# Kernel tuning notes

Hardware: AMD Instinct MI355X
Metric: run time of the kernel (lower is better)

## Reference

```python
import jax, jax.numpy as jnp
import numpy as np

B, T_ENC, E, T_DEC, N_MELS, H, A = 32, 256, 512, 200, 80, 1024, 128


def setup_inputs() -> dict:
    key = jax.random.key(0)
    ks = jax.random.split(key, 20)
    rn = lambda k, s, sc: (jax.random.normal(k, s, jnp.float32) * sc)
    return {
        "inputs": rn(ks[0], (B, T_ENC, E), 1.0),
        "padded_mels": rn(ks[1], (B, N_MELS, T_DEC), 1.0),
        "W_enc": rn(ks[2], (E, A), 0.04),
        "W_q": rn(ks[3], (H, A), 0.03),
        "conv_w": rn(ks[4], (32, 1, 31), 0.18),
        "conv_b": jnp.zeros((32,), jnp.float32),
        "W_loc": rn(ks[5], (32, A), 0.18),
        "v_e": rn(ks[6], (A,), 0.09),
        "pw1": rn(ks[7], (N_MELS, 256), 0.11),
        "pb1": jnp.zeros((256,), jnp.float32),
        "pw2": rn(ks[8], (256, 256), 0.06),
        "pb2": jnp.zeros((256,), jnp.float32),
        "Wi1": rn(ks[9], (256 + E, 4 * H), 0.03),
        "Wh1": rn(ks[10], (H, 4 * H), 0.03),
        "bl1": jnp.zeros((4 * H,), jnp.float32),
        "Wi2": rn(ks[11], (H, 4 * H), 0.03),
        "Wh2": rn(ks[12], (H, 4 * H), 0.03),
        "bl2": jnp.zeros((4 * H,), jnp.float32),
        "Wp": rn(ks[13], (H + E, N_MELS), 0.025),
        "bp": jnp.zeros((N_MELS,), jnp.float32),
    }


def _lstm_cell(x, h, c, Wi, Wh, b):
    g = x @ Wi + h @ Wh + b
    i, f, gg, o = jnp.split(g, 4, axis=-1)
    c = jax.nn.sigmoid(f) * c + jax.nn.sigmoid(i) * jnp.tanh(gg)
    h = jax.nn.sigmoid(o) * jnp.tanh(c)
    return h, c


def reference(inputs, padded_mels, W_enc, W_q, conv_w, conv_b, W_loc, v_e,
              pw1, pb1, pw2, pb2, Wi1, Wh1, bl1, Wi2, Wh2, bl2, Wp, bp):
    b, t_enc, e = inputs.shape
    n_mels, t_dec = padded_mels.shape[1], padded_mels.shape[2]
    proc_enc = inputs @ W_enc  # [B, T_enc, A]
    # teacher forcing: prepend go frame, use frames 0..T_dec-1 as inputs
    go = jnp.zeros((b, n_mels, 1), inputs.dtype)
    prev_mels = jnp.moveaxis(jnp.concatenate([go, padded_mels], axis=-1)[:, :, :-1], -1, 0)  # [T_dec,B,80]

    def step(carry, prev_mel):
        h1, c1, h2, c2, ctx, aw_cum = carry
        # prenet (dropout omitted: eval/deterministic reference)
        x = jax.nn.relu(prev_mel @ pw1 + pb1)
        x = jax.nn.relu(x @ pw2 + pb2)
        # 2-layer LSTM on [prenet, prev context]
        lstm_in = jnp.concatenate([x, ctx], axis=-1)
        h1n, c1n = _lstm_cell(lstm_in, h1, c1, Wi1, Wh1, bl1)
        h2n, c2n = _lstm_cell(h1n, h2, c2, Wi2, Wh2, bl2)
        # location-sensitive attention
        q = h2n @ W_q  # [B, A]
        loc = jax.lax.conv_general_dilated(aw_cum[:, None, :], conv_w, (1,), "SAME",
                                           dimension_numbers=("NCH", "OIH", "NCH"))
        loc = loc + conv_b[None, :, None]
        loc = jnp.swapaxes(loc, 1, 2) @ W_loc  # [B, T_enc, A]
        energies = jnp.tanh(q[:, None, :] + loc + proc_enc) @ v_e  # [B, T_enc]
        aw = jax.nn.softmax(energies, axis=1)
        ctx_n = jnp.einsum("bt,bte->be", aw, inputs)
        out = jnp.concatenate([h2n, ctx_n], axis=-1) @ Wp + bp  # [B, 80]
        return (h1n, c1n, h2n, c2n, ctx_n, aw_cum + aw), out

    z = lambda *s: jnp.zeros(s, inputs.dtype)
    carry0 = (z(b, H), z(b, H), z(b, H), z(b, H), z(b, e), z(b, t_enc))
    _, mels = jax.lax.scan(step, carry0, prev_mels)
    return mels  # [T_dec, B, 80]
```

## Files before the change

kernel.cpp:

```cpp
#include <hip/hip_runtime.h>
#include <hip/hip_fp16.h>

#define BB   32
#define TENC 256
#define EE   512
#define TDEC 200
#define NM   80
#define HH   1024
#define AA   128
#define GG   4096
#define K1   1792
#define K2   2048

#define NGRP  16
#define GRPSZ 16

typedef _Float16 h8v  __attribute__((ext_vector_type(8)));
typedef float    f32x4 __attribute__((ext_vector_type(4)));

__device__ __forceinline__ float sigf(float x){ return 1.0f/(1.0f + __expf(-x)); }
__device__ __forceinline__ float tanhfast(float x){ return 1.0f - 2.0f/(1.0f + __expf(2.0f*x)); }

__device__ __forceinline__ unsigned short h2b(float f){
    _Float16 h = (_Float16)f; unsigned short u; __builtin_memcpy(&u, &h, 2); return u;
}
__device__ __forceinline__ void st64(unsigned long long* p, unsigned long long v){
    __hip_atomic_store(p, v, __ATOMIC_RELAXED, __HIP_MEMORY_SCOPE_AGENT);
}
__device__ __forceinline__ void st32(unsigned int* p, unsigned int v){
    __hip_atomic_store(p, v, __ATOMIC_RELAXED, __HIP_MEMORY_SCOPE_AGENT);
}
__device__ __forceinline__ unsigned long long ld64(const unsigned long long* p){
    return __hip_atomic_load(p, __ATOMIC_RELAXED, __HIP_MEMORY_SCOPE_AGENT);
}
__device__ __forceinline__ unsigned int ld32(const unsigned int* p){
    return __hip_atomic_load(p, __ATOMIC_RELAXED, __HIP_MEMORY_SCOPE_AGENT);
}


__global__ void k_zero(float* __restrict__ p, int n){
    int i = blockIdx.x*blockDim.x + threadIdx.x;
    if(i < n) p[i] = 0.f;
}

__global__ void k_cvt_half(const float* __restrict__ src, __half* __restrict__ dst, int n){
    int i = blockIdx.x*blockDim.x + threadIdx.x;
    int stride = gridDim.x*blockDim.x;
    for(; i<n; i+=stride) dst[i] = __float2half(src[i]);
}

__global__ __launch_bounds__(256) void k_transpose2(const float* __restrict__ src,
                                                    _Float16* __restrict__ dst,
                                                    int K, int C, int dstStride, int kOff, int pack){
    __shared__ float tile[32][33];
    const int tid = threadIdx.x;
    const int c0 = blockIdx.x*32, k0 = blockIdx.y*32;
    const int cl = tid & 31, r8 = tid >> 5;
    #pragma unroll
    for(int i=0;i<4;i++){
        const int k = k0 + r8 + i*8;
        if(k < K && c0+cl < C) tile[r8 + i*8][cl] = src[(size_t)k*C + c0 + cl];
    }
    __syncthreads();
    const int kl = tid & 31, c8 = tid >> 5;
    #pragma unroll
    for(int i=0;i<4;i++){
        const int c = c0 + c8 + i*8;
        if(c < C && k0+kl < K){
            const int p = pack ? ((c & 1023)*4 + (c >> 10)) : c;
            dst[(size_t)p*dstStride + kOff + k0 + kl] = (_Float16)tile[kl][c8 + i*8];
        }
    }
}

__global__ __launch_bounds__(256) void k_wfrag(const _Float16* __restrict__ WT,
                                               _Float16* __restrict__ WF, int K){
    const int tid = threadIdx.x;
    const int l = tid & 63, f = tid >> 6;
    const int ct = blockIdx.y;
    const int kc = blockIdx.x*4 + f;
    const h8v v = *(const h8v*)(WT + (size_t)(ct*16 + (l & 15))*K + kc*32 + ((l >> 4) << 3));
    *(h8v*)(WF + ((size_t)(ct*(K >> 5) + kc)*64 + l)*8) = v;
}

__global__ __launch_bounds__(128) void k_proc_enc(const float* __restrict__ inputs,
                                                  const float* __restrict__ Wenc,
                                                  __half* __restrict__ pe_h){
    const int row = blockIdx.x;
    const int a   = threadIdx.x;
    const float* in = inputs + (size_t)row*EE;
    float acc = 0.f;
    for(int k=0;k<EE;k++) acc = fmaf(in[k], Wenc[k*AA + a], acc);
    pe_h[(size_t)row*AA + a] = __float2half(acc);
}

__global__ __launch_bounds__(320) void k_pip(const float* __restrict__ inputs,
                                             const float* __restrict__ Wp_c,
                                             __half* __restrict__ PIP){
    const int b = blockIdx.x >> 6, t4 = (blockIdx.x & 63)*4;
    __shared__ float xs[4*EE];
    const int tid = threadIdx.x;
    for(int i=tid; i<4*EE; i+=320) xs[i] = inputs[((size_t)b*TENC + t4)*EE + i];
    __syncthreads();
    const int tl = tid/80, m = tid%80;
    float acc = 0.f;
    for(int k=0;k<EE;k++) acc = fmaf(xs[tl*EE + k], Wp_c[k*NM + m], acc);
    PIP[((size_t)b*TENC + t4 + tl)*NM + m] = __float2half(acc);
}

__global__ __launch_bounds__(256) void k_prenet(const float* __restrict__ pmels,
                                                const float* __restrict__ pw1, const float* __restrict__ pb1,
                                                const float* __restrict__ pw2, const float* __restrict__ pb2,
                                                _Float16* __restrict__ XS1h){
    const int t = blockIdx.x;
    __shared__ float pm[BB*NM];
    __shared__ float h1s[BB*256];
    const int tid = threadIdx.x;
    for(int el=tid; el<BB*NM; el+=256){
        const int b = el/NM, m = el%NM;
        pm[el] = (t==0) ? 0.f : pmels[(size_t)(b*NM + m)*TDEC + (t-1)];
    }
    __syncthreads();
    const int a = tid;
    float acc[BB];
    #pragma unroll
    for(int b=0;b<BB;b++) acc[b]=0.f;
    for(int m=0;m<NM;m++){
        const float w = pw1[m*256 + a];
        #pragma unroll
        for(int b=0;b<BB;b++) acc[b] = fmaf(pm[b*NM+m], w, acc[b]);
    }
    {
        const float bias = pb1[a];
        for(int b=0;b<BB;b++) h1s[b*256+a] = fmaxf(acc[b]+bias, 0.f);
    }
    __syncthreads();
    #pragma unroll
    for(int b=0;b<BB;b++) acc[b]=0.f;
    for(int k=0;k<256;k++){
        const float w = pw2[k*256 + a];
        #pragma unroll
        for(int b=0;b<BB;b++) acc[b] = fmaf(h1s[b*256+k], w, acc[b]);
    }
    {
        const float bias = pb2[a];
        #pragma unroll
        for(int b=0;b<BB;b++)
            XS1h[((size_t)t*BB + b)*K1 + a] = (_Float16)fmaxf(acc[b]+bias, 0.f);
    }
}

__global__ void k_mloc(const float* __restrict__ conv_w, const float* __restrict__ conv_b,
                       const float* __restrict__ W_loc, float* __restrict__ Mloc, float* __restrict__ cbp){
    const int a = threadIdx.x;
    for(int d=0; d<31; d++){
        float s = 0.f;
        for(int ch=0; ch<32; ch++) s = fmaf(conv_w[ch*31 + d], W_loc[ch*AA + a], s);
        Mloc[d*AA + a] = s;
    }
    float s = 0.f;
    for(int ch=0; ch<32; ch++) s = fmaf(conv_b[ch], W_loc[ch*AA + a], s);
    cbp[a] = s;
}


__device__ __forceinline__ void gridbar(unsigned int* bb, unsigned int bi, int tid, int bid, int& dead){
    __syncthreads();
    if(tid == 0){
        const int g = bid >> 4;
        unsigned int v = __hip_atomic_fetch_add(&bb[g*32], 1u, __ATOMIC_RELAXED, __HIP_MEMORY_SCOPE_AGENT);
        if(v == bi*GRPSZ - 1u)
            __hip_atomic_fetch_add(&bb[512], 1u, __ATOMIC_RELAXED, __HIP_MEMORY_SCOPE_AGENT);
        if(!dead){
            unsigned int guard = 0;
            if((bid & 15) == 0){
                while(ld32(&bb[512]) < bi*NGRP){
                    __builtin_amdgcn_s_sleep(2);
                    if(++guard > 3000000u){ dead = 1; break; }
                }
                #pragma unroll
                for(int m=1; m<GRPSZ; m++) st32(&bb[576 + (bid+m)*32], bi);
            } else {
                while(ld32(&bb[576 + bid*32]) < bi){
                    __builtin_amdgcn_s_sleep(2);
                    if(++guard > 3000000u){ dead = 1; break; }
                }
            }
        }
    }
    __syncthreads();
}

template<int LF, bool AGENT>
__device__ __forceinline__ void gemm_win(f32x4& accL, f32x4& accH,
    const _Float16* __restrict__ aCol, int strideA,
    const _Float16* __restrict__ bWave, int l)
{
    const int r = l & 15;
    const _Float16* a0 = aCol + (size_t)r*strideA + ((l >> 4) << 3);
    #pragma unroll
    for(int j=0;j<LF;j++){
        const h8v b8 = *(const h8v*)(bWave + (size_t)j*512);
        h8v aL, aH;
        if constexpr(AGENT){
            union { unsigned long long u[2]; h8v v; } uL, uH;
            const unsigned long long* pL = (const unsigned long long*)(a0 + j*32);
            const unsigned long long* pH = (const unsigned long long*)(a0 + (size_t)16*strideA + j*32);
            uL.u[0] = ld64(pL);   uL.u[1] = ld64(pL+1);
            uH.u[0] = ld64(pH);   uH.u[1] = ld64(pH+1);
            aL = uL.v; aH = uH.v;
        } else {
            aL = *(const h8v*)(a0 + j*32);
            aH = *(const h8v*)(a0 + (size_t)16*strideA + j*32);
        }
        accL = __builtin_amdgcn_mfma_f32_16x16x32_f16(aL, b8, accL, 0, 0, 0);
        accH = __builtin_amdgcn_mfma_f32_16x16x32_f16(aH, b8, accH, 0, 0, 0);
    }
}

__device__ __forceinline__ void lstm_finish(
    const f32x4& accL, const f32x4& accH,
    const float* __restrict__ bias, float& cv,
    _Float16* __restrict__ hDst, int strideH,
    float* part, float* stage, int tid, int bid, int l, int kw)
{
    {
        const int r0 = (l >> 4) << 2, c = l & 15;
        #pragma unroll
        for(int j=0;j<4;j++){
            part[(kw*32 + r0 + j)*18 + c]      = accL[j];
            part[(kw*32 + 16 + r0 + j)*18 + c] = accH[j];
        }
    }
    __syncthreads();
    if(tid < 128){
        const int b = tid & 31, cl = tid >> 5;
        float g[4];
        #pragma unroll
        for(int gi=0; gi<4; gi++){
            const int c2 = cl*4 + gi;
            float s = 0.f;
            #pragma unroll
            for(int q=0;q<8;q++) s += part[(q*32 + b)*18 + c2];
            const int p = bid*16 + c2;
            g[gi] = s + bias[(p & 3)*HH + (p >> 2)];
        }
        const float cn = sigf(g[1])*cv + sigf(g[0])*tanhfast(g[2]);
        cv = cn;
        stage[tid] = sigf(g[3])*tanhfast(cn);
    }
    __syncthreads();
    if(tid < 32){
        const int b = tid;
        unsigned long long pk =
              (unsigned long long)h2b(stage[0*32+b])
            | ((unsigned long long)h2b(stage[1*32+b]) << 16)
            | ((unsigned long long)h2b(stage[2*32+b]) << 32)
            | ((unsigned long long)h2b(stage[3*32+b]) << 48);
        st64((unsigned long long*)(hDst + (size_t)b*strideH + bid*4), pk);
    }
}

__global__ __launch_bounds__(512) void k_decode(
    _Float16* __restrict__ XS1h, _Float16* __restrict__ H2P,
    const _Float16* __restrict__ W1F, const _Float16* __restrict__ W2F,
    const float* __restrict__ bl1, const float* __restrict__ bl2,
    const _Float16* __restrict__ WqT, const float* __restrict__ cbp,
    const float* __restrict__ Mloc, const float* __restrict__ ve,
    const __half* __restrict__ pe,
    const __half* __restrict__ inputs_h, const __half* __restrict__ PIP,
    const _Float16* __restrict__ WohT, const float* __restrict__ bp,
    float* __restrict__ out, unsigned int* __restrict__ bar)
{
    const int tid = threadIdx.x, bid = blockIdx.x;
    const int l = tid & 63, kw = tid >> 6;

    __shared__ float s_ml[31*AA];
    __shared__ float s_ves[AA];
    __shared__ float s_part[8*32*18];
    __shared__ float s_h2s[1024];
    __shared__ float s_qc[4*AA];
    __shared__ float s_qf[AA];
    __shared__ float s_awin[288];
    __shared__ float s_aw[TENC];
    __shared__ float s_awc[TENC];
    __shared__ float s_red1[320];
    __shared__ float s_red2[320];
    __shared__ float s_sred[8];

    for(int i=tid; i<31*AA; i+=512) s_ml[i] = Mloc[i];
    if(tid < AA) s_ves[tid] = ve[tid];
    if(bid < BB) for(int i=tid; i<TENC; i+=512) s_awc[i] = 0.f;
    __syncthreads();

    float c1v = 0.f, c2v = 0.f;
    int dead = 0;
    unsigned int bi = 0;

    const f32x4 z4 = {0.f,0.f,0.f,0.f};
    f32x4 p1L = z4, p1H = z4;
    f32x4 p2L = z4, p2H = z4;

    gemm_win<1,false>(p1L,p1H, XS1h + kw*32,        K1, W1F + ((size_t)(bid*56 + kw)*64 + l)*8, l);
    gemm_win<4,false>(p1L,p1H, XS1h + 768 + kw*128, K1, W1F + ((size_t)(bid*56 + 24 + kw*4)*64 + l)*8, l);
    gemm_win<4,true >(p2L,p2H, H2P + (size_t)BB*HH + kw*128, HH, W2F + ((size_t)(bid*64 + 32 + kw*4)*64 + l)*8, l);

    for(int t=0; t<TDEC; t++){
        _Float16* rowT  = XS1h + (size_t)t*BB*K1;
        _Float16* rowT1 = XS1h + (size_t)(t+1)*BB*K1;
        _Float16* h2cur = H2P + (size_t)(t & 1)*BB*HH;

        {
            f32x4 aL = p1L, aH = p1H;
            gemm_win<2,false>(aL,aH, rowT + 256 + kw*64, K1, W1F + ((size_t)(bid*56 + 8 + kw*2)*64 + l)*8, l);
            lstm_finish(aL,aH, bl1, c1v, rowT1 + 768, K1, s_part, s_qf, tid, bid, l, kw);
        }
        gridbar(bar, ++bi, tid, bid, dead);

        {
            f32x4 aL = p2L, aH = p2H;
            gemm_win<4,false>(aL,aH, rowT1 + 768 + kw*128, K1, W2F + ((size_t)(bid*64 + kw*4)*64 + l)*8, l);
            lstm_finish(aL,aH, bl2, c2v, h2cur, HH, s_part, s_qf, tid, bid, l, kw);
        }
        gridbar(bar, ++bi, tid, bid, dead);

        p1L = z4; p1H = z4; p2L = z4; p2H = z4;
        gemm_win<1,false>(p1L,p1H, rowT1 + kw*32,        K1, W1F + ((size_t)(bid*56 + kw)*64 + l)*8, l);
        gemm_win<4,false>(p1L,p1H, rowT1 + 768 + kw*128, K1, W1F + ((size_t)(bid*56 + 24 + kw*4)*64 + l)*8, l);
        gemm_win<4,true >(p2L,p2H, h2cur + kw*128,       HH, W2F + ((size_t)(bid*64 + 32 + kw*4)*64 + l)*8, l);

        if(bid < BB){
            const int b = bid;
            {
                const unsigned int* hp = (const unsigned int*)(h2cur + (size_t)b*HH);
                union { unsigned int u; _Float16 h[2]; } cu;
                cu.u = ld32(hp + tid);
                s_h2s[2*tid]   = (float)cu.h[0];
                s_h2s[2*tid+1] = (float)cu.h[1];
            }
            for(int i=tid; i<286; i+=512){
                const int g2 = i - 15;
                s_awin[i] = (g2>=0 && g2<TENC) ? s_awc[g2] : 0.f;
            }
            __syncthreads();
            {
                const int a = tid & 127, tp = tid >> 7;
                float qa = 0.f;
                const _Float16* wq = WqT + (size_t)a*HH + tp*256;
                const float* hs = s_h2s + tp*256;
                for(int kb=0; kb<256; kb+=8){
                    const h8v w8 = *(const h8v*)(wq + kb);
                    #pragma unroll
                    for(int i2=0;i2<8;i2++) qa = fmaf((float)w8[i2], hs[kb+i2], qa);
                }
                s_qc[tp*AA + a] = qa;
            }
            __syncthreads();
            if(tid < AA) s_qf[tid] = s_qc[tid] + s_qc[AA+tid] + s_qc[2*AA+tid] + s_qc[3*AA+tid] + cbp[tid];
            __syncthreads();
            float* s_ep = s_part;
            #pragma unroll
            for(int it=0; it<2; it++){
                const int ti = tid & 255, ah = (tid >> 8) + 2*it;
                const int a0 = ah*32;
                float s[32];
                const h8v* pp = (const h8v*)((const _Float16*)pe + ((size_t)(b*TENC + ti))*AA + a0);
                #pragma unroll
                for(int vq=0; vq<4; vq++){
                    const h8v pv = pp[vq];
                    #pragma unroll
                    for(int j=0;j<8;j++) s[vq*8+j] = s_qf[a0+vq*8+j] + (float)pv[j];
                }
                for(int d=0; d<31; d++){
                    const float w = s_awin[ti+d];
                    #pragma unroll
                    for(int j=0;j<32;j++) s[j] = fmaf(w, s_ml[d*AA + a0 + j], s[j]);
                }
                float es = 0.f;
                #pragma unroll
                for(int j=0;j<32;j++) es = fmaf(tanhfast(s[j]), s_ves[a0+j], es);
                s_ep[ah*256 + ti] = es;
            }
            __syncthreads();
            float e = -1e30f;
            if(tid < 256) e = s_ep[tid] + s_ep[256+tid] + s_ep[512+tid] + s_ep[768+tid];
            float m_ = e;
            #pragma unroll
            for(int o=32;o>=1;o>>=1) m_ = fmaxf(m_, __shfl_xor(m_, o));
            if((tid&63)==0 && tid<256) s_sred[tid>>6] = m_;
            __syncthreads();
            const float mm = fmaxf(fmaxf(s_sred[0],s_sred[1]), fmaxf(s_sred[2],s_sred[3]));
            const float pv2 = (tid<256) ? __expf(e - mm) : 0.f;
            float sum = pv2;
            #pragma unroll
            for(int o=32;o>=1;o>>=1) sum += __shfl_xor(sum, o);
            if((tid&63)==0 && tid<256) s_sred[4+(tid>>6)] = sum;
            __syncthreads();
            sum = s_sred[4]+s_sred[5]+s_sred[6]+s_sred[7];
            if(tid < 256){
                const float awv = pv2/sum;
                s_aw[tid] = awv;
                s_awc[tid] += awv;
            }
            __syncthreads();
            float* ctxred = s_part;
            {
                const int ch8 = tid & 63, tq = tid >> 6;
                const _Float16* ib = (const _Float16*)inputs_h + (size_t)b*TENC*EE + ch8*8;
                float a_[8];
                #pragma unroll
                for(int j=0;j<8;j++) a_[j]=0.f;
                for(int tt=tq; tt<TENC; tt+=8){
                    const float wv = s_aw[tt];
                    const h8v x8 = *(const h8v*)(ib + (size_t)tt*EE);
                    #pragma unroll
                    for(int j=0;j<8;j++) a_[j] = fmaf(wv, (float)x8[j], a_[j]);
                }
                #pragma unroll
                for(int j=0;j<8;j++) ctxred[tq*512 + ch8*8 + j] = a_[j];
            }
            __syncthreads();
            if(tid < 256){
                const int ch = 2*tid;
                float s0=0.f, s1=0.f;
                #pragma unroll
                for(int q=0;q<8;q++){ s0 += ctxred[q*512 + ch]; s1 += ctxred[q*512 + ch + 1]; }
                union { unsigned int u; _Float16 h[2]; } cu;
                cu.h[0] = (_Float16)s0; cu.h[1] = (_Float16)s1;
                st32((unsigned int*)(rowT1 + (size_t)b*K1 + 256) + tid, cu.u);
            }
            if(tid < 320){
                const int m2 = tid % 80, kh = tid / 80;
                float s1 = 0.f;
                const _Float16* wo = WohT + (size_t)m2*HH + kh*256;
                const float* hs = s_h2s + kh*256;
                for(int kb=0; kb<256; kb+=8){
                    const h8v w8 = *(const h8v*)(wo + kb);
                    #pragma unroll
                    for(int i2=0;i2<8;i2++) s1 = fmaf((float)w8[i2], hs[kb+i2], s1);
                }
                s_red1[kh*80 + m2] = s1;
                float s2 = 0.f;
                const __half* pp2 = PIP + ((size_t)(b*TENC) + kh*64)*NM + m2;
                const float* awp = s_aw + kh*64;
                for(int tt=0; tt<64; tt++)
                    s2 = fmaf(awp[tt], __half2float(pp2[(size_t)tt*NM]), s2);
                s_red2[kh*80 + m2] = s2;
            }
            __syncthreads();
            if(tid < NM){
                const float o = s_red1[tid]+s_red1[80+tid]+s_red1[160+tid]+s_red1[240+tid]
                              + s_red2[tid]+s_red2[80+tid]+s_red2[160+tid]+s_red2[240+tid] + bp[tid];
                out[((size_t)t*BB + b)*NM + tid] = o;
            }
        }
        gridbar(bar, ++bi, tid, bid, dead);
    }
}


extern "C" void kernel_launch(void* const* d_in, const int* in_sizes, int n_in,
                              void* d_out, int out_size, void* d_ws, size_t ws_size,
                              hipStream_t stream)
{
    const float* inputs = (const float*)d_in[0];
    const float* pmels  = (const float*)d_in[1];
    const float* W_enc  = (const float*)d_in[2];
    const float* W_q    = (const float*)d_in[3];
    const float* conv_w = (const float*)d_in[4];
    const float* conv_b = (const float*)d_in[5];
    const float* W_loc  = (const float*)d_in[6];
    const float* v_e    = (const float*)d_in[7];
    const float* pw1    = (const float*)d_in[8];
    const float* pb1    = (const float*)d_in[9];
    const float* pw2    = (const float*)d_in[10];
    const float* pb2    = (const float*)d_in[11];
    const float* Wi1    = (const float*)d_in[12];
    const float* Wh1    = (const float*)d_in[13];
    const float* bl1    = (const float*)d_in[14];
    const float* Wi2    = (const float*)d_in[15];
    const float* Wh2    = (const float*)d_in[16];
    const float* bl2    = (const float*)d_in[17];
    const float* Wp     = (const float*)d_in[18];
    const float* bp     = (const float*)d_in[19];
    float* out = (float*)d_out;
    (void)in_sizes; (void)n_in; (void)out_size; (void)ws_size;

    char* ws = (char*)d_ws;
    size_t off = 0;
    auto carve = [&](size_t bytes)->char* {
        char* p = ws + off;
        off += (bytes + 255) & ~(size_t)255;
        return p;
    };
    __half*    inputs_h = (__half*)   carve((size_t)BB*TENC*EE*2);
    __half*    pe_h     = (__half*)   carve((size_t)BB*TENC*AA*2);
    __half*    PIP      = (__half*)   carve((size_t)BB*TENC*NM*2);
    _Float16*  XS1h     = (_Float16*) carve((size_t)(TDEC+1)*BB*K1*2);
    _Float16*  H2P      = (_Float16*) carve((size_t)2*BB*HH*2);
    _Float16*  WA       = (_Float16*) carve((size_t)GG*K2*2);
    _Float16*  WB       = (_Float16*) carve((size_t)GG*K1*2);
    _Float16*  W2F      = (_Float16*) carve((size_t)GG*K2*2);
    _Float16*  WqT      = (_Float16*) carve((size_t)AA*HH*2);
    _Float16*  WohT     = (_Float16*) carve((size_t)NM*HH*2);
    const int NBAR = 576 + 256*32;
    unsigned int* bar   = (unsigned int*)carve((size_t)NBAR*4);
    float* Mloc = (float*)carve((size_t)31*AA*4);
    float* cbp  = (float*)carve((size_t)AA*4);
    _Float16* W1F = WA;

    k_zero<<<(NBAR+255)/256,256,0,stream>>>((float*)bar, NBAR);
    k_zero<<<(2*BB*HH/2+255)/256,256,0,stream>>>((float*)H2P, 2*BB*HH/2);
    k_zero<<<(BB*K1/2+255)/256,256,0,stream>>>((float*)XS1h, BB*K1/2);
    k_cvt_half<<<2048,256,0,stream>>>(inputs, inputs_h, BB*TENC*EE);
    k_proc_enc<<<BB*TENC,128,0,stream>>>(inputs, W_enc, pe_h);
    k_prenet<<<TDEC,256,0,stream>>>(pmels, pw1,pb1,pw2,pb2, XS1h);
    k_mloc<<<1,128,0,stream>>>(conv_w, conv_b, W_loc, Mloc, cbp);
    k_transpose2<<<dim3(GG/32, 1024/32),256,0,stream>>>(Wi2, WA, 1024, GG, K2, 0,    1);
    k_transpose2<<<dim3(GG/32, 1024/32),256,0,stream>>>(Wh2, WA, 1024, GG, K2, 1024, 1);
    k_wfrag<<<dim3(K2/128, GG/16),256,0,stream>>>(WA, W2F, K2);
    k_transpose2<<<dim3(GG/32,  768/32),256,0,stream>>>(Wi1, WB, 768,  GG, K1, 0,    1);
    k_transpose2<<<dim3(GG/32, 1024/32),256,0,stream>>>(Wh1, WB, 1024, GG, K1, 768,  1);
    k_wfrag<<<dim3(K1/128, GG/16),256,0,stream>>>(WB, W1F, K1);
    k_transpose2<<<dim3(AA/32, 1024/32),256,0,stream>>>(W_q, WqT, 1024, AA, HH, 0,   0);
    k_transpose2<<<dim3(3,     1024/32),256,0,stream>>>(Wp,  WohT, 1024, NM, HH, 0,  0);
    k_pip<<<BB*64,320,0,stream>>>(inputs, Wp + (size_t)HH*NM, PIP);

    {
        void* ka[17];
        ka[0]  = (void*)&XS1h;
        ka[1]  = (void*)&H2P;
        ka[2]  = (void*)&W1F;
        ka[3]  = (void*)&W2F;
        ka[4]  = (void*)&bl1;
        ka[5]  = (void*)&bl2;
        ka[6]  = (void*)&WqT;
        ka[7]  = (void*)&cbp;
        ka[8]  = (void*)&Mloc;
        ka[9]  = (void*)&v_e;
        ka[10] = (void*)&pe_h;
        ka[11] = (void*)&inputs_h;
        ka[12] = (void*)&PIP;
        ka[13] = (void*)&WohT;
        ka[14] = (void*)&bp;
        ka[15] = (void*)&out;
        ka[16] = (void*)&bar;
        hipLaunchCooperativeKernel((const void*)k_decode, dim3(256), dim3(512),
                                   ka, 0, stream);
    }
}
```

Before: 11.36 ms.

## Replace atomic grid barrier with flag-based hierarchical barrier and spinning waves

Replaces the atomic-counter grid barrier with per-block flag stores. Group leaders poll their 15 members' flags, publish a group flag, then poll all 16 group flags before releasing members, with no sleep between polls. The other waves of each block busy-spin on a shared-memory flag, doing dummy FMAs, instead of waiting at __syncthreads. The aim is lower barrier latency from avoiding atomics and sleeps, at the cost of more memory polling traffic, extra power draw from the spinning, and a shorter deadlock guard.

```diff
diff --git a/kernel.cpp b/kernel.cpp
--- a/kernel.cpp
+++ b/kernel.cpp
@@ -164,28 +164,45 @@
 }
 
 
-__device__ __forceinline__ void gridbar(unsigned int* bb, unsigned int bi, int tid, int bid, int& dead){
+__device__ __forceinline__ void gridbar(unsigned int* bb, volatile unsigned int* s_go,
+                                        unsigned int bi, int tid, int bid, int& dead){
     __syncthreads();
     if(tid == 0){
-        const int g = bid >> 4;
-        unsigned int v = __hip_atomic_fetch_add(&bb[g*32], 1u, __ATOMIC_RELAXED, __HIP_MEMORY_SCOPE_AGENT);
-        if(v == bi*GRPSZ - 1u)
-            __hip_atomic_fetch_add(&bb[512], 1u, __ATOMIC_RELAXED, __HIP_MEMORY_SCOPE_AGENT);
+        st32(&bb[bid*32], bi);
         if(!dead){
             unsigned int guard = 0;
             if((bid & 15) == 0){
-                while(ld32(&bb[512]) < bi*NGRP){
-                    __builtin_amdgcn_s_sleep(2);
-                    if(++guard > 3000000u){ dead = 1; break; }
+                const int g = bid >> 4;
+                for(;;){
+                    int ok = 1;
+                    #pragma unroll
+                    for(int m=1; m<GRPSZ; m++) ok &= (ld32(&bb[(bid+m)*32]) >= bi);
+                    if(ok) break;
+                    if(++guard > 400000u){ dead = 1; break; }
+                }
+                st32(&bb[(256+g)*32], bi);
+                for(;;){
+                    int ok = 1;
+                    #pragma unroll
+                    for(int q=0; q<NGRP; q++) ok &= (ld32(&bb[(256+q)*32]) >= bi);
+                    if(ok) break;
+                    if(++guard > 400000u){ dead = 1; break; }
                 }
                 #pragma unroll
-                for(int m=1; m<GRPSZ; m++) st32(&bb[576 + (bid+m)*32], bi);
+                for(int m=1; m<GRPSZ; m++) st32(&bb[(bid+m)*32 + 1], bi);
             } else {
-                while(ld32(&bb[576 + bid*32]) < bi){
-                    __builtin_amdgcn_s_sleep(2);
-                    if(++guard > 3000000u){ dead = 1; break; }
-                }
-            }
+                while(ld32(&bb[bid*32 + 1]) < bi){
+                    if(++guard > 400000u){ dead = 1; break; }
+                }
+            }
+        }
+        *s_go = bi;
+    } else if(tid >= 64){
+        float x = (float)tid;
+        while(*s_go < bi){
+            #pragma unroll
+            for(int i=0;i<32;i++) x = fmaf(x, 1.0000001f, 1e-30f);
+            asm volatile("" : "+v"(x));
         }
     }
     __syncthreads();
@@ -287,10 +304,12 @@
     __shared__ float s_red1[320];
     __shared__ float s_red2[320];
     __shared__ float s_sred[8];
+    __shared__ unsigned int s_go;
 
     for(int i=tid; i<31*AA; i+=512) s_ml[i] = Mloc[i];
     if(tid < AA) s_ves[tid] = ve[tid];
     if(bid < BB) for(int i=tid; i<TENC; i+=512) s_awc[i] = 0.f;
+    if(tid == 0) s_go = 0;
     __syncthreads();
 
     float c1v = 0.f, c2v = 0.f;
@@ -315,14 +334,14 @@
             gemm_win<2,false>(aL,aH, rowT + 256 + kw*64, K1, W1F + ((size_t)(bid*56 + 8 + kw*2)*64 + l)*8, l);
             lstm_finish(aL,aH, bl1, c1v, rowT1 + 768, K1, s_part, s_qf, tid, bid, l, kw);
         }
-        gridbar(bar, ++bi, tid, bid, dead);
+        gridbar(bar, &s_go, ++bi, tid, bid, dead);
 
         {
             f32x4 aL = p2L, aH = p2H;
             gemm_win<4,false>(aL,aH, rowT1 + 768 + kw*128, K1, W2F + ((size_t)(bid*64 + kw*4)*64 + l)*8, l);
             lstm_finish(aL,aH, bl2, c2v, h2cur, HH, s_part, s_qf, tid, bid, l, kw);
         }
-        gridbar(bar, ++bi, tid, bid, dead);
+        gridbar(bar, &s_go, ++bi, tid, bid, dead);
 
         p1L = z4; p1H = z4; p2L = z4; p2H = z4;
         gemm_win<1,false>(p1L,p1H, rowT1 + kw*32,        K1, W1F + ((size_t)(bid*56 + kw)*64 + l)*8, l);
@@ -454,7 +473,7 @@
                 out[((size_t)t*BB + b)*NM + tid] = o;
             }
         }
-        gridbar(bar, ++bi, tid, bid, dead);
+        gridbar(bar, &s_go, ++bi, tid, bid, dead);
     }
 }
 
@@ -503,7 +522,7 @@
     _Float16*  W2F      = (_Float16*) carve((size_t)GG*K2*2);
     _Float16*  WqT      = (_Float16*) carve((size_t)AA*HH*2);
     _Float16*  WohT     = (_Float16*) carve((size_t)NM*HH*2);
-    const int NBAR = 576 + 256*32;
+    const int NBAR = (256 + NGRP)*32;
     unsigned int* bar   = (unsigned int*)carve((size_t)NBAR*4);
     float* Mloc = (float*)carve((size_t)31*AA*4);
     float* cbp  = (float*)carve((size_t)AA*4);
```

Measured after the change: 15.16 ms. +33.4%, slower.
